# Optimization experiments

Measured on AMD Instinct MI355X. Metric: run time of the kernel, lower is better.

## Reference

```python
import jax, jax.numpy as jnp
import numpy as np

N_NODES = 100000
N_EDGES = 1600000
IN_CH = 128
HID = 128
NUM_CLASSES = 10
NUM_GRAPHS = 128
SLOPE = 0.01  # F.leaky_relu default negative_slope


def _lin_params(key, fan_in, fan_out):
    kw, kb = jax.random.split(key)
    bound = 1.0 / np.sqrt(fan_in)
    W = jax.random.uniform(kw, (fan_in, fan_out), jnp.float32, -bound, bound)
    b = jax.random.uniform(kb, (fan_out,), jnp.float32, -bound, bound)
    return W, b


def setup_inputs() -> dict:
    key = jax.random.key(0)
    ks = jax.random.split(key, 8)
    x = jax.random.normal(ks[0], (N_NODES, IN_CH), jnp.float32)
    edge_index = jax.random.randint(ks[1], (2, N_EDGES), 0, N_NODES, jnp.int64)
    batch = jnp.sort(jax.random.randint(ks[2], (N_NODES,), 0, NUM_GRAPHS, jnp.int64))
    W1, b1 = _lin_params(ks[3], IN_CH, HID)
    W2, b2 = _lin_params(ks[4], HID, HID)
    W3, b3 = _lin_params(ks[5], HID, HID // 2)
    W4, b4 = _lin_params(ks[6], HID // 2, HID // 2)
    W5, b5 = _lin_params(ks[7], HID // 2, NUM_CLASSES)
    return {"x": x, "edge_index": edge_index, "batch": batch,
            "W1": W1, "b1": b1, "W2": W2, "b2": b2,
            "W3": W3, "b3": b3, "W4": W4, "b4": b4, "W5": W5, "b5": b5}


def gcn_conv(x, src, dst, W, b):
    # PyG GCNConv: h = x W; add self-loops; symmetric norm D^-1/2 (A+I) D^-1/2
    h = x @ W  # [N, F]
    n = x.shape[0]
    deg = jnp.zeros((n,), h.dtype).at[dst].add(1.0) + 1.0  # includes self-loop
    dinv = jax.lax.rsqrt(deg)
    norm = dinv[src] * dinv[dst]  # [E]
    agg = jnp.zeros_like(h).at[dst].add(h[src] * norm[:, None])
    agg = agg + h * (dinv * dinv)[:, None]  # self-loop term: 1/deg
    return agg + b


def reference(x, edge_index, batch, W1, b1, W2, b2, W3, b3, W4, b4, W5, b5):
    src, dst = edge_index[0], edge_index[1]
    h = jax.nn.leaky_relu(gcn_conv(x, src, dst, W1, b1), SLOPE)
    h = jax.nn.leaky_relu(gcn_conv(h, src, dst, W2, b2), SLOPE)
    # global mean pool over graphs
    sums = jax.ops.segment_sum(h, batch, num_segments=NUM_GRAPHS)
    cnts = jax.ops.segment_sum(jnp.ones((h.shape[0],), h.dtype), batch,
                               num_segments=NUM_GRAPHS)
    g = sums / jnp.maximum(cnts, 1.0)[:, None]  # [NUM_GRAPHS, HID]
    g = jax.nn.leaky_relu(g @ W3 + b3, SLOPE)
    g = jax.nn.leaky_relu(g @ W4 + b4, SLOPE)
    return g @ W5 + b5
```

## Files before the change

kernel.cpp:

```cpp
#include <hip/hip_runtime.h>
#include <hip/hip_bf16.h>


#define SLOPE 0.01f

__device__ __forceinline__ float lrelu(float x) { return x > 0.f ? x : SLOPE * x; }

__device__ __forceinline__ unsigned short f2bf(float f) {
    union { float f; unsigned u; } v; v.f = f;
    unsigned r = v.u + 0x7fffu + ((v.u >> 16) & 1u);
    return (unsigned short)(r >> 16);
}
__device__ __forceinline__ float bf2f(unsigned short h) {
    union { unsigned u; float f; } v; v.u = ((unsigned)h) << 16;
    return v.f;
}
__device__ __forceinline__ float bf_lo(unsigned x) {
    union { unsigned u; float f; } v; v.u = x << 16; return v.f;
}
__device__ __forceinline__ float bf_hi(unsigned x) {
    union { unsigned u; float f; } v; v.u = x & 0xffff0000u; return v.f;
}
__device__ __forceinline__ unsigned packbf(float lo, float hi) {
    return (unsigned)f2bf(lo) | ((unsigned)f2bf(hi) << 16);
}

typedef __attribute__((ext_vector_type(8))) short bf16x8;
typedef __attribute__((ext_vector_type(4))) float f32x4;
typedef __attribute__((ext_vector_type(2))) float f32x2;

#define LDA 136
#define CAPP 5120
#define MAXBUCK 400

__global__ void k_init(int* __restrict__ zbase, int nz,
                       const float* __restrict__ W1, unsigned short* __restrict__ WT1,
                       const float* __restrict__ W2, unsigned short* __restrict__ WT2) {
    int b = blockIdx.x;
    if (b < 64) {
        int idx = b * 256 + threadIdx.x;
        int k = idx >> 7, n = idx & 127;
        WT1[n * 128 + k] = f2bf(W1[idx]);
    } else if (b < 128) {
        int idx = (b - 64) * 256 + threadIdx.x;
        int k = idx >> 7, n = idx & 127;
        WT2[n * 128 + k] = f2bf(W2[idx]);
    } else {
        int i = (b - 128) * 256 + threadIdx.x;
        if (i < nz) zbase[i] = 0;
    }
}

template<bool IN_BF16, bool SCALE>
__device__ __forceinline__ void gemm_body(const void* __restrict__ Xv,
                                          const unsigned short* __restrict__ WT,
                                          unsigned short* __restrict__ Y, int M,
                                          unsigned short* Bs, int bid,
                                          const float* __restrict__ dinvg) {
    int t = threadIdx.x;
    int row0 = bid * 64;
    int w = t >> 6, l = t & 63;
    int lr = l & 15;
    int ko = (l >> 4) * 8;

    int gr = row0 + w * 16 + lr;
    bool inb = gr < M;
    bf16x8 afr[4];
    if (IN_BF16) {
        const unsigned short* Xrow = (const unsigned short*)Xv + (size_t)gr * 128;
#pragma unroll
        for (int kc = 0; kc < 4; ++kc) {
            if (inb) afr[kc] = *(const bf16x8*)&Xrow[kc * 32 + ko];
            else     afr[kc] = (bf16x8){0, 0, 0, 0, 0, 0, 0, 0};
        }
    } else {
        const float* Xrow = (const float*)Xv + (size_t)gr * 128;
#pragma unroll
        for (int kc = 0; kc < 4; ++kc) {
            if (inb) {
                float4 u0 = *(const float4*)&Xrow[kc * 32 + ko];
                float4 u1 = *(const float4*)&Xrow[kc * 32 + ko + 4];
                union { bf16x8 v; unsigned u[4]; } cv;
                cv.u[0] = packbf(u0.x, u0.y);
                cv.u[1] = packbf(u0.z, u0.w);
                cv.u[2] = packbf(u1.x, u1.y);
                cv.u[3] = packbf(u1.z, u1.w);
                afr[kc] = cv.v;
            } else afr[kc] = (bf16x8){0, 0, 0, 0, 0, 0, 0, 0};
        }
    }

    {
        const uint4* WT4 = (const uint4*)WT;
#pragma unroll
        for (int i = 0; i < 8; ++i) {
            int idx = t + i * 256;
            int n = idx >> 4, c8 = idx & 15;
            *(uint4*)&Bs[n * LDA + c8 * 8] = WT4[idx];
        }
    }
    __syncthreads();

    f32x4 acc[8];
#pragma unroll
    for (int c = 0; c < 8; ++c) acc[c] = (f32x4){0.f, 0.f, 0.f, 0.f};

#pragma unroll
    for (int kc = 0; kc < 4; ++kc) {
        int kb = kc * 32 + ko;
        bf16x8 bfr[8];
#pragma unroll
        for (int ct = 0; ct < 8; ++ct)
            bfr[ct] = *(const bf16x8*)&Bs[(ct * 16 + lr) * LDA + kb];
#pragma unroll
        for (int ct = 0; ct < 8; ++ct)
            acc[ct] = __builtin_amdgcn_mfma_f32_16x16x32_bf16(afr[kc], bfr[ct], acc[ct], 0, 0, 0);
    }

    __syncthreads();
    int qr = (l >> 4) * 4;
#pragma unroll
    for (int i = 0; i < 4; ++i) {
        int r = w * 16 + qr + i;
        float sc = 1.f;
        if (SCALE) {
            int gr2 = row0 + r;
            sc = (gr2 < M) ? dinvg[gr2] : 1.f;
        }
#pragma unroll
        for (int ct = 0; ct < 8; ++ct)
            Bs[r * LDA + ct * 16 + lr] = f2bf(acc[ct][i] * sc);
    }
    __syncthreads();
    {
        uint4* Y4 = (uint4*)Y;
#pragma unroll
        for (int i = 0; i < 4; ++i) {
            int idx = t + i * 256;
            int r = idx >> 4, c8 = idx & 15;
            int g2 = row0 + r;
            if (g2 < M) Y4[(size_t)g2 * 16 + c8] = *(const uint4*)&Bs[r * LDA + c8 * 8];
        }
    }
}

__device__ __forceinline__ void p1_body(const int* __restrict__ src,
                                        const int* __restrict__ dst,
                                        int E, int nb, int* __restrict__ g_cnt,
                                        unsigned* __restrict__ part,
                                        int* hist, int bid) {
    int* base = hist + MAXBUCK;
    int t = threadIdx.x;
    for (int b = t; b < nb; b += 256) hist[b] = 0;
    __syncthreads();
    int e0b = bid * 4096;
#pragma unroll
    for (int j = 0; j < 4; ++j) {
        int e = e0b + j * 1024 + t * 4;
        if (e + 3 < E) {
            int4 d = *(const int4*)&dst[e];
            atomicAdd(&hist[d.x >> 8], 1);
            atomicAdd(&hist[d.y >> 8], 1);
            atomicAdd(&hist[d.z >> 8], 1);
            atomicAdd(&hist[d.w >> 8], 1);
        } else {
            for (int k = e; k < E && k < e + 4; ++k)
                atomicAdd(&hist[dst[k] >> 8], 1);
        }
    }
    __syncthreads();
    for (int b = t; b < nb; b += 256) {
        int c = hist[b];
        base[b] = c ? atomicAdd(&g_cnt[b], c) : 0;
        hist[b] = 0;
    }
    __syncthreads();
#pragma unroll
    for (int j = 0; j < 4; ++j) {
        int e = e0b + j * 1024 + t * 4;
        if (e + 3 < E) {
            int4 d = *(const int4*)&dst[e];
            int4 s = *(const int4*)&src[e];
            int bk, p;
            bk = d.x >> 8; p = base[bk] + atomicAdd(&hist[bk], 1);
            if (p < CAPP) part[(size_t)bk * CAPP + p] = ((unsigned)s.x << 8) | ((unsigned)d.x & 255u);
            bk = d.y >> 8; p = base[bk] + atomicAdd(&hist[bk], 1);
            if (p < CAPP) part[(size_t)bk * CAPP + p] = ((unsigned)s.y << 8) | ((unsigned)d.y & 255u);
            bk = d.z >> 8; p = base[bk] + atomicAdd(&hist[bk], 1);
            if (p < CAPP) part[(size_t)bk * CAPP + p] = ((unsigned)s.z << 8) | ((unsigned)d.z & 255u);
            bk = d.w >> 8; p = base[bk] + atomicAdd(&hist[bk], 1);
            if (p < CAPP) part[(size_t)bk * CAPP + p] = ((unsigned)s.w << 8) | ((unsigned)d.w & 255u);
        } else {
            for (int k = e; k < E && k < e + 4; ++k) {
                int bk = dst[k] >> 8;
                int p = base[bk] + atomicAdd(&hist[bk], 1);
                if (p < CAPP) part[(size_t)bk * CAPP + p] = ((unsigned)src[k] << 8) | ((unsigned)dst[k] & 255u);
            }
        }
    }
}

__global__ __launch_bounds__(256) void k_p1_gemm1(
    const int* __restrict__ src, const int* __restrict__ dst, int E, int nb,
    int* __restrict__ g_cnt, unsigned* __restrict__ part, int nbP1,
    const float* __restrict__ X, const unsigned short* __restrict__ WT,
    unsigned short* __restrict__ Y, int M) {
    __shared__ __align__(16) unsigned short Bs[128 * LDA];
    int b = blockIdx.x;
    if (b < nbP1) p1_body(src, dst, E, nb, g_cnt, part, (int*)Bs, b);
    else gemm_body<false, false>((const void*)X, WT, Y, M, Bs, b - nbP1, nullptr);
}

__global__ __launch_bounds__(256) void k_p2(const unsigned* __restrict__ part,
                                            const int* __restrict__ g_cnt,
                                            int* __restrict__ csr,
                                            int* __restrict__ rp0, int* __restrict__ rp1,
                                            float* __restrict__ dinvg,
                                            unsigned short* __restrict__ H, int N) {
    __shared__ int cnt[256];
    __shared__ int sc[256];
    __shared__ float dvl[256];
    int b = blockIdx.x, t = threadIdx.x;
    int nbase = b << 8;
    int nn = N - nbase; if (nn > 256) nn = 256;

    cnt[t] = 0;
    __syncthreads();

    int Eb = g_cnt[b]; if (Eb > CAPP) Eb = CAPP;
    const unsigned* pp = part + (size_t)b * CAPP;
    for (int i = t; i < Eb; i += 256)
        atomicAdd(&cnt[pp[i] & 255u], 1);
    __syncthreads();

    int v = cnt[t];
    sc[t] = v;
    __syncthreads();
    for (int off = 1; off < 256; off <<= 1) {
        int add = (t >= off) ? sc[t - off] : 0;
        __syncthreads();
        sc[t] += add;
        __syncthreads();
    }
    int excl = sc[t] - v;

    float di = rsqrtf((float)v + 1.0f);
    if (t < nn) {
        rp0[nbase + t] = b * CAPP + excl;
        rp1[nbase + t] = b * CAPP + excl + v;
        dinvg[nbase + t] = di;
    }
    dvl[t] = di;
    cnt[t] = excl;
    __syncthreads();

    for (int i = t; i < Eb; i += 256) {
        unsigned pv = pp[i];
        int lcl = pv & 255u;
        int p = atomicAdd(&cnt[lcl], 1);
        csr[(size_t)b * CAPP + p] = (int)(pv >> 8);
    }

    uint4* H4 = (uint4*)H;
    int tot = nn * 16;
    for (int i = t; i < tot; i += 256) {
        int r = i >> 4, c = i & 15;
        float d = dvl[r];
        uint4 hv = H4[(size_t)(nbase + r) * 16 + c];
        uint4 o;
        o.x = packbf(bf_lo(hv.x) * d, bf_hi(hv.x) * d);
        o.y = packbf(bf_lo(hv.y) * d, bf_hi(hv.y) * d);
        o.z = packbf(bf_lo(hv.z) * d, bf_hi(hv.z) * d);
        o.w = packbf(bf_lo(hv.w) * d, bf_hi(hv.w) * d);
        H4[(size_t)(nbase + r) * 16 + c] = o;
    }
}

__global__ __launch_bounds__(256) void k_gemm2(
    const void* __restrict__ Xv, const unsigned short* __restrict__ WT,
    unsigned short* __restrict__ Y, int M, const float* __restrict__ dinvg) {
    __shared__ __align__(16) unsigned short Bs[128 * LDA];
    gemm_body<true, true>(Xv, WT, Y, M, Bs, blockIdx.x, dinvg);
}

__device__ __forceinline__ void acc8(f32x2& S0, f32x2& S1, f32x2& S2, f32x2& S3,
                                     uint4 hv) {
    f32x2 t;
    t.x = bf_lo(hv.x); t.y = bf_hi(hv.x); S0 += t;
    t.x = bf_lo(hv.y); t.y = bf_hi(hv.y); S1 += t;
    t.x = bf_lo(hv.z); t.y = bf_hi(hv.z); S2 += t;
    t.x = bf_lo(hv.w); t.y = bf_hi(hv.w); S3 += t;
}

__global__ __launch_bounds__(256) void k_agg6(const unsigned short* __restrict__ H,
                                              const int* __restrict__ csr,
                                              const int* __restrict__ rp0,
                                              const int* __restrict__ rp1,
                                              const float* __restrict__ dinvg,
                                              const float* __restrict__ bias,
                                              unsigned short* __restrict__ OUT, int N) {
    int l = threadIdx.x & 63;
    int u = blockIdx.x * 4 + (threadIdx.x >> 6);
    if (u >= N) return;
    int g = l >> 4, cl = l & 15;
    int e0 = rp0[u], e1 = rp1[u];
    const uint4* H4 = (const uint4*)H;

    f32x2 A0 = {0.f, 0.f}, A1 = {0.f, 0.f}, A2 = {0.f, 0.f}, A3 = {0.f, 0.f};
    f32x2 B0 = {0.f, 0.f}, B1 = {0.f, 0.f}, B2 = {0.f, 0.f}, B3 = {0.f, 0.f};

    int e = e0 + g;
    int cA = 0, cB = 0, cC = 0, cD = 0;
    if (e < e1)      cA = csr[e];
    if (e + 4 < e1)  cB = csr[e + 4];
    if (e + 8 < e1)  cC = csr[e + 8];
    if (e + 12 < e1) cD = csr[e + 12];
    while (e < e1) {
        int uA = cA, uB = cB, uC = cC, uD = cD;
        bool dB = (e + 4) < e1, dC = (e + 8) < e1, dD = (e + 12) < e1;
        int en = e + 16;
        if (en < e1)      cA = csr[en];
        if (en + 4 < e1)  cB = csr[en + 4];
        if (en + 8 < e1)  cC = csr[en + 8];
        if (en + 12 < e1) cD = csr[en + 12];
        uint4 hA, hB, hC, hD;
        hA = H4[(size_t)uA * 16 + cl];
        if (dB) hB = H4[(size_t)uB * 16 + cl];
        if (dC) hC = H4[(size_t)uC * 16 + cl];
        if (dD) hD = H4[(size_t)uD * 16 + cl];
        acc8(A0, A1, A2, A3, hA);
        if (dB) acc8(B0, B1, B2, B3, hB);
        if (dC) acc8(A0, A1, A2, A3, hC);
        if (dD) acc8(B0, B1, B2, B3, hD);
        e = en;
    }
    A0 += B0; A1 += B1; A2 += B2; A3 += B3;
    float a0 = A0.x, a1 = A0.y, a2 = A1.x, a3 = A1.y;
    float a4 = A2.x, a5 = A2.y, a6 = A3.x, a7 = A3.y;

    a0 += __shfl_xor(a0, 16); a0 += __shfl_xor(a0, 32);
    a1 += __shfl_xor(a1, 16); a1 += __shfl_xor(a1, 32);
    a2 += __shfl_xor(a2, 16); a2 += __shfl_xor(a2, 32);
    a3 += __shfl_xor(a3, 16); a3 += __shfl_xor(a3, 32);
    a4 += __shfl_xor(a4, 16); a4 += __shfl_xor(a4, 32);
    a5 += __shfl_xor(a5, 16); a5 += __shfl_xor(a5, 32);
    a6 += __shfl_xor(a6, 16); a6 += __shfl_xor(a6, 32);
    a7 += __shfl_xor(a7, 16); a7 += __shfl_xor(a7, 32);

    if (g == 0) {
        uint4 hs = H4[(size_t)u * 16 + cl];
        a0 += bf_lo(hs.x); a1 += bf_hi(hs.x);
        a2 += bf_lo(hs.y); a3 += bf_hi(hs.y);
        a4 += bf_lo(hs.z); a5 += bf_hi(hs.z);
        a6 += bf_lo(hs.w); a7 += bf_hi(hs.w);
        float du = dinvg[u];
        float4 c0 = *(const float4*)&bias[cl * 8];
        float4 c1 = *(const float4*)&bias[cl * 8 + 4];
        uint4 o;
        o.x = packbf(lrelu(a0 * du + c0.x), lrelu(a1 * du + c0.y));
        o.y = packbf(lrelu(a2 * du + c0.z), lrelu(a3 * du + c0.w));
        o.z = packbf(lrelu(a4 * du + c1.x), lrelu(a5 * du + c1.y));
        o.w = packbf(lrelu(a6 * du + c1.z), lrelu(a7 * du + c1.w));
        ((uint4*)OUT)[(size_t)u * 16 + cl] = o;
    }
}

#define PCH 128
__global__ __launch_bounds__(256) void k_pool3(const unsigned short* __restrict__ H,
                                               const int* __restrict__ batch,
                                               float* __restrict__ Gsum,
                                               int* __restrict__ Gcnt, int N) {
    int t = threadIdx.x;
    int st = t >> 6, c2 = t & 63;
    int n0 = blockIdx.x * PCH + st * (PCH / 4);
    int n1 = n0 + (PCH / 4); if (n1 > N) n1 = N;
    if (n0 >= N) return;
    float a0 = 0.f, a1 = 0.f;
    int cur = batch[n0], runstart = n0;
    for (int n = n0; n < n1; ++n) {
        int g = batch[n];
        if (g != cur) {
            atomicAdd(&Gsum[cur * 128 + c2 * 2], a0);
            atomicAdd(&Gsum[cur * 128 + c2 * 2 + 1], a1);
            if (c2 == 0) atomicAdd(&Gcnt[cur], n - runstart);
            a0 = a1 = 0.f; cur = g; runstart = n;
        }
        unsigned hv = *(const unsigned*)&H[(size_t)n * 128 + c2 * 2];
        a0 += bf_lo(hv); a1 += bf_hi(hv);
    }
    atomicAdd(&Gsum[cur * 128 + c2 * 2], a0);
    atomicAdd(&Gsum[cur * 128 + c2 * 2 + 1], a1);
    if (c2 == 0) atomicAdd(&Gcnt[cur], n1 - runstart);
}

__global__ __launch_bounds__(64) void k_mlp(const float* __restrict__ Gsum,
                                            const int* __restrict__ Gcnt,
                                            const float* __restrict__ W3, const float* __restrict__ b3,
                                            const float* __restrict__ W4, const float* __restrict__ b4,
                                            const float* __restrict__ W5, const float* __restrict__ b5,
                                            float* __restrict__ OUT) {
    __shared__ float row[128];
    __shared__ float t1[64];
    __shared__ float t2[64];
    int g = blockIdx.x, t = threadIdx.x;
    float inv = 1.0f / fmaxf((float)Gcnt[g], 1.0f);
    row[t]      = Gsum[g * 128 + t] * inv;
    row[t + 64] = Gsum[g * 128 + t + 64] * inv;
    __syncthreads();
    float acc = b3[t];
    for (int k = 0; k < 128; ++k) acc += row[k] * W3[k * 64 + t];
    t1[t] = lrelu(acc);
    __syncthreads();
    acc = b4[t];
    for (int k = 0; k < 64; ++k) acc += t1[k] * W4[k * 64 + t];
    t2[t] = lrelu(acc);
    __syncthreads();
    if (t < 10) {
        acc = b5[t];
        for (int k = 0; k < 64; ++k) acc += t2[k] * W5[k * 10 + t];
        OUT[g * 10 + t] = acc;
    }
}


extern "C" void kernel_launch(void* const* d_in, const int* in_sizes, int n_in,
                              void* d_out, int out_size, void* d_ws, size_t ws_size,
                              hipStream_t stream) {
    const float* x    = (const float*)d_in[0];
    const int*   ei   = (const int*)d_in[1];
    const int*   batch= (const int*)d_in[2];
    const float* W1   = (const float*)d_in[3];
    const float* b1   = (const float*)d_in[4];
    const float* W2   = (const float*)d_in[5];
    const float* b2   = (const float*)d_in[6];
    const float* W3   = (const float*)d_in[7];
    const float* b3   = (const float*)d_in[8];
    const float* W4   = (const float*)d_in[9];
    const float* b4   = (const float*)d_in[10];
    const float* W5   = (const float*)d_in[11];
    const float* b5   = (const float*)d_in[12];
    float* out = (float*)d_out;

    const int N = in_sizes[2];
    const int E = in_sizes[1] / 2;
    const int NG = 128;

    const int* src = ei;
    const int* dst = ei + E;

    char* w = (char*)d_ws;
    unsigned short* bufA = (unsigned short*)w; w += (size_t)N * 128 * 2;
    unsigned short* bufB = (unsigned short*)w; w += (size_t)N * 128 * 2;
    int*   g_cnt = (int*)w;   w += 512 * 4;
    float* gsum  = (float*)w; w += (size_t)NG * 128 * 4;
    int*   gcnt  = (int*)w;   w += (size_t)NG * 4;
    float* dinv  = (float*)w; w += (size_t)N * 4;
    int*   rp0   = (int*)w;   w += (size_t)N * 4;
    int*   rp1   = (int*)w;   w += (size_t)N * 4;
    unsigned* part = (unsigned*)w; w += (size_t)MAXBUCK * CAPP * 4;
    int*   csr   = (int*)w;   w += (size_t)MAXBUCK * CAPP * 4;
    unsigned short* WT1 = (unsigned short*)w; w += 128 * 128 * 2;
    unsigned short* WT2 = (unsigned short*)w; w += 128 * 128 * 2;
    (void)ws_size; (void)n_in; (void)out_size;

    int nbB  = (N + 255) >> 8;
    int nbP1 = (E + 4095) / 4096;
    int nbG  = (N + 63) / 64;
    int nZero = 512 + NG * 128 + NG;
    int nbZ  = (nZero + 255) / 256;

    k_init<<<128 + nbZ, 256, 0, stream>>>(g_cnt, nZero, W1, WT1, W2, WT2);
    k_p1_gemm1<<<nbP1 + nbG, 256, 0, stream>>>(src, dst, E, nbB, g_cnt, part,
                                               nbP1, x, WT1, bufA, N);
    k_p2<<<nbB, 256, 0, stream>>>(part, g_cnt, csr, rp0, rp1, dinv, bufA, N);

    int nbA = (N + 3) / 4;

    k_agg6<<<nbA, 256, 0, stream>>>(bufA, csr, rp0, rp1, dinv, b1, bufB, N);
    k_gemm2<<<nbG, 256, 0, stream>>>(bufB, WT2, bufA, N, dinv);
    k_agg6<<<nbA, 256, 0, stream>>>(bufA, csr, rp0, rp1, dinv, b2, bufB, N);

    int nbP = (N + PCH - 1) / PCH;
    k_pool3<<<nbP, 256, 0, stream>>>(bufB, batch, gsum, gcnt, N);
    k_mlp<<<NG, 64, 0, stream>>>(gsum, gcnt, W3, b3, W4, b4, W5, b5, out);
}
```

Measured before the change: 339.1 us.

## Aggregate each node with a 16-lane group using shuffled neighbor indices

The aggregation kernel moves from one 64-lane wavefront per node (four edge groups, then a cross-group shuffle reduction) to one 16-lane group per node, with 16 nodes per block. Each group loads up to 16 CSR indices at once and broadcasts them with width-16 shuffles, then gathers the neighbour rows four at a time. This drops the cross-lane reduction and the idle lanes in the final write. Row pointers are packed into a single int2 array so each node needs one load. The catch is less memory-level parallelism per node, since edges are now walked serially within a group.

```diff
diff --git a/kernel.cpp b/kernel.cpp
--- a/kernel.cpp
+++ b/kernel.cpp
@@ -214,7 +214,7 @@
 __global__ __launch_bounds__(256) void k_p2(const unsigned* __restrict__ part,
                                             const int* __restrict__ g_cnt,
                                             int* __restrict__ csr,
-                                            int* __restrict__ rp0, int* __restrict__ rp1,
+                                            int2* __restrict__ rpz,
                                             float* __restrict__ dinvg,
                                             unsigned short* __restrict__ H, int N) {
     __shared__ int cnt[256];
@@ -246,8 +246,7 @@
 
     float di = rsqrtf((float)v + 1.0f);
     if (t < nn) {
-        rp0[nbase + t] = b * CAPP + excl;
-        rp1[nbase + t] = b * CAPP + excl + v;
+        rpz[nbase + t] = make_int2(b * CAPP + excl, b * CAPP + excl + v);
         dinvg[nbase + t] = di;
     }
     dvl[t] = di;
@@ -292,77 +291,66 @@
     t.x = bf_lo(hv.w); t.y = bf_hi(hv.w); S3 += t;
 }
 
-__global__ __launch_bounds__(256) void k_agg6(const unsigned short* __restrict__ H,
+__global__ __launch_bounds__(256) void k_agg7(const unsigned short* __restrict__ H,
                                               const int* __restrict__ csr,
-                                              const int* __restrict__ rp0,
-                                              const int* __restrict__ rp1,
+                                              const int2* __restrict__ rpz,
                                               const float* __restrict__ dinvg,
                                               const float* __restrict__ bias,
                                               unsigned short* __restrict__ OUT, int N) {
-    int l = threadIdx.x & 63;
-    int u = blockIdx.x * 4 + (threadIdx.x >> 6);
+    int t = threadIdx.x;
+    int grp = t >> 4, cl = t & 15;
+    int u = blockIdx.x * 16 + grp;
     if (u >= N) return;
-    int g = l >> 4, cl = l & 15;
-    int e0 = rp0[u], e1 = rp1[u];
     const uint4* H4 = (const uint4*)H;
+
+    int2 rz = rpz[u];
+    int e0 = rz.x, e1 = rz.y;
+    uint4 hs = H4[(size_t)u * 16 + cl];
+    float du = dinvg[u];
 
     f32x2 A0 = {0.f, 0.f}, A1 = {0.f, 0.f}, A2 = {0.f, 0.f}, A3 = {0.f, 0.f};
     f32x2 B0 = {0.f, 0.f}, B1 = {0.f, 0.f}, B2 = {0.f, 0.f}, B3 = {0.f, 0.f};
 
-    int e = e0 + g;
-    int cA = 0, cB = 0, cC = 0, cD = 0;
-    if (e < e1)      cA = csr[e];
-    if (e + 4 < e1)  cB = csr[e + 4];
-    if (e + 8 < e1)  cC = csr[e + 8];
-    if (e + 12 < e1) cD = csr[e + 12];
+    int e = e0;
     while (e < e1) {
-        int uA = cA, uB = cB, uC = cC, uD = cD;
-        bool dB = (e + 4) < e1, dC = (e + 8) < e1, dD = (e + 12) < e1;
-        int en = e + 16;
-        if (en < e1)      cA = csr[en];
-        if (en + 4 < e1)  cB = csr[en + 4];
-        if (en + 8 < e1)  cC = csr[en + 8];
-        if (en + 12 < e1) cD = csr[en + 12];
-        uint4 hA, hB, hC, hD;
-        hA = H4[(size_t)uA * 16 + cl];
-        if (dB) hB = H4[(size_t)uB * 16 + cl];
-        if (dC) hC = H4[(size_t)uC * 16 + cl];
-        if (dD) hD = H4[(size_t)uD * 16 + cl];
-        acc8(A0, A1, A2, A3, hA);
-        if (dB) acc8(B0, B1, B2, B3, hB);
-        if (dC) acc8(A0, A1, A2, A3, hC);
-        if (dD) acc8(B0, B1, B2, B3, hD);
-        e = en;
-    }
+        int nn = e1 - e; if (nn > 16) nn = 16;
+        int ci = (cl < nn) ? csr[e + cl] : 0;
+        int j = 0;
+        for (; j + 4 <= nn; j += 4) {
+            int i0 = __shfl(ci, j,     16);
+            int i1 = __shfl(ci, j + 1, 16);
+            int i2 = __shfl(ci, j + 2, 16);
+            int i3 = __shfl(ci, j + 3, 16);
+            uint4 hA = H4[(size_t)i0 * 16 + cl];
+            uint4 hB = H4[(size_t)i1 * 16 + cl];
+            uint4 hC = H4[(size_t)i2 * 16 + cl];
+            uint4 hD = H4[(size_t)i3 * 16 + cl];
+            acc8(A0, A1, A2, A3, hA);
+            acc8(B0, B1, B2, B3, hB);
+            acc8(A0, A1, A2, A3, hC);
+            acc8(B0, B1, B2, B3, hD);
+        }
+        for (; j < nn; ++j) {
+            int i0 = __shfl(ci, j, 16);
+            uint4 hA = H4[(size_t)i0 * 16 + cl];
+            acc8(A0, A1, A2, A3, hA);
+        }
+        e += nn;
+    }
+
+    acc8(A0, A1, A2, A3, hs);
     A0 += B0; A1 += B1; A2 += B2; A3 += B3;
     float a0 = A0.x, a1 = A0.y, a2 = A1.x, a3 = A1.y;
     float a4 = A2.x, a5 = A2.y, a6 = A3.x, a7 = A3.y;
 
-    a0 += __shfl_xor(a0, 16); a0 += __shfl_xor(a0, 32);
-    a1 += __shfl_xor(a1, 16); a1 += __shfl_xor(a1, 32);
-    a2 += __shfl_xor(a2, 16); a2 += __shfl_xor(a2, 32);
-    a3 += __shfl_xor(a3, 16); a3 += __shfl_xor(a3, 32);
-    a4 += __shfl_xor(a4, 16); a4 += __shfl_xor(a4, 32);
-    a5 += __shfl_xor(a5, 16); a5 += __shfl_xor(a5, 32);
-    a6 += __shfl_xor(a6, 16); a6 += __shfl_xor(a6, 32);
-    a7 += __shfl_xor(a7, 16); a7 += __shfl_xor(a7, 32);
-
-    if (g == 0) {
-        uint4 hs = H4[(size_t)u * 16 + cl];
-        a0 += bf_lo(hs.x); a1 += bf_hi(hs.x);
-        a2 += bf_lo(hs.y); a3 += bf_hi(hs.y);
-        a4 += bf_lo(hs.z); a5 += bf_hi(hs.z);
-        a6 += bf_lo(hs.w); a7 += bf_hi(hs.w);
-        float du = dinvg[u];
-        float4 c0 = *(const float4*)&bias[cl * 8];
-        float4 c1 = *(const float4*)&bias[cl * 8 + 4];
-        uint4 o;
-        o.x = packbf(lrelu(a0 * du + c0.x), lrelu(a1 * du + c0.y));
-        o.y = packbf(lrelu(a2 * du + c0.z), lrelu(a3 * du + c0.w));
-        o.z = packbf(lrelu(a4 * du + c1.x), lrelu(a5 * du + c1.y));
-        o.w = packbf(lrelu(a6 * du + c1.z), lrelu(a7 * du + c1.w));
-        ((uint4*)OUT)[(size_t)u * 16 + cl] = o;
-    }
+    float4 c0 = *(const float4*)&bias[cl * 8];
+    float4 c1 = *(const float4*)&bias[cl * 8 + 4];
+    uint4 o;
+    o.x = packbf(lrelu(a0 * du + c0.x), lrelu(a1 * du + c0.y));
+    o.y = packbf(lrelu(a2 * du + c0.z), lrelu(a3 * du + c0.w));
+    o.z = packbf(lrelu(a4 * du + c1.x), lrelu(a5 * du + c1.y));
+    o.w = packbf(lrelu(a6 * du + c1.z), lrelu(a7 * du + c1.w));
+    ((uint4*)OUT)[(size_t)u * 16 + cl] = o;
 }
 
 #define PCH 128
@@ -455,8 +443,7 @@
     float* gsum  = (float*)w; w += (size_t)NG * 128 * 4;
     int*   gcnt  = (int*)w;   w += (size_t)NG * 4;
     float* dinv  = (float*)w; w += (size_t)N * 4;
-    int*   rp0   = (int*)w;   w += (size_t)N * 4;
-    int*   rp1   = (int*)w;   w += (size_t)N * 4;
+    int2*  rpz   = (int2*)w;  w += (size_t)N * 8;
     unsigned* part = (unsigned*)w; w += (size_t)MAXBUCK * CAPP * 4;
     int*   csr   = (int*)w;   w += (size_t)MAXBUCK * CAPP * 4;
     unsigned short* WT1 = (unsigned short*)w; w += 128 * 128 * 2;
@@ -472,13 +459,13 @@
     k_init<<<128 + nbZ, 256, 0, stream>>>(g_cnt, nZero, W1, WT1, W2, WT2);
     k_p1_gemm1<<<nbP1 + nbG, 256, 0, stream>>>(src, dst, E, nbB, g_cnt, part,
                                                nbP1, x, WT1, bufA, N);
-    k_p2<<<nbB, 256, 0, stream>>>(part, g_cnt, csr, rp0, rp1, dinv, bufA, N);
-
-    int nbA = (N + 3) / 4;
-
-    k_agg6<<<nbA, 256, 0, stream>>>(bufA, csr, rp0, rp1, dinv, b1, bufB, N);
+    k_p2<<<nbB, 256, 0, stream>>>(part, g_cnt, csr, rpz, dinv, bufA, N);
+
+    int nbA = (N + 15) / 16;
+
+    k_agg7<<<nbA, 256, 0, stream>>>(bufA, csr, rpz, dinv, b1, bufB, N);
     k_gemm2<<<nbG, 256, 0, stream>>>(bufB, WT2, bufA, N, dinv);
-    k_agg6<<<nbA, 256, 0, stream>>>(bufA, csr, rp0, rp1, dinv, b2, bufB, N);
+    k_agg7<<<nbA, 256, 0, stream>>>(bufA, csr, rpz, dinv, b2, bufB, N);
 
     int nbP = (N + PCH - 1) / PCH;
     k_pool3<<<nbP, 256, 0, stream>>>(bufB, batch, gsum, gcnt, N);
```

Measured after the change: 332.4 us. About the same (-2.0%).
